# Optimization experiments

Hardware: AMD Instinct MI355X
Metric: run time of the kernel (lower is better)

## Reference

```python
import jax, jax.numpy as jnp
import numpy as np
import math

B, S, D, NH = 2, 2048, 1024, 16
DK = D // NH
E, TOPK, MOE_H, NSH = 8, 2, 1024, 2
SH_H = MOE_H * NSH
EPS = 1e-6


def setup_inputs() -> dict:
    key = jax.random.key(0)
    ks = jax.random.split(key, 24)
    p = lambda k, shape: jax.random.normal(k, shape, jnp.float32) * 0.02
    x = jax.random.normal(ks[0], (B, S, D), jnp.float32)
    # RoPE tables: freqs_cis = exp(i * t * theta^{-2j/dk}), passed as cos/sin
    inv = 1.0 / (10000.0 ** (np.arange(0, DK, 2, dtype=np.float32) / DK))
    ang = np.outer(np.arange(S, dtype=np.float32), inv)
    freqs_cos = jnp.asarray(np.cos(ang), jnp.float32)
    freqs_sin = jnp.asarray(np.sin(ang), jnp.float32)
    mask = jnp.triu(jnp.full((S, S), -1e9, jnp.float32), k=1)  # causal additive mask
    return {
        'x': x, 'freqs_cos': freqs_cos, 'freqs_sin': freqs_sin, 'mask': mask,
        'wq': p(ks[1], (D, D)), 'wk': p(ks[2], (D, D)),
        'wv': p(ks[3], (D, D)), 'wo': p(ks[4], (D, D)),
        'attn_norm_w': jnp.ones((D,), jnp.float32),
        'ffn_norm_w': jnp.ones((D,), jnp.float32),
        'gate_w': p(ks[5], (E, D)), 'gate_b': p(ks[6], (E,)),
        'w1': p(ks[7], (E, MOE_H, D)), 'b1': p(ks[8], (E, MOE_H)),
        'w2': p(ks[9], (E, D, MOE_H)), 'b2': p(ks[10], (E, D)),
        'w3': p(ks[11], (E, MOE_H, D)), 'b3': p(ks[12], (E, MOE_H)),
        'sg_w': p(ks[13], (SH_H, D)), 'su_w': p(ks[14], (SH_H, D)),
        'sd_w': p(ks[15], (D, SH_H)),
    }


def rmsnorm(x, w):
    f = x.astype(jnp.float32)
    y = f * jax.lax.rsqrt(jnp.mean(f * f, axis=-1, keepdims=True) + EPS)
    return y.astype(x.dtype) * w


def rope(t, cos, sin):
    # t: [b, s, h, dk]; pairs (t[2j], t[2j+1]) as complex, multiplied by e^{i ang}
    tr, ti = t[..., 0::2], t[..., 1::2]
    c, s = cos[None, :, None, :], sin[None, :, None, :]
    outr = tr * c - ti * s
    outi = tr * s + ti * c
    return jnp.stack([outr, outi], axis=-1).reshape(t.shape)


def reference(x, freqs_cos, freqs_sin, mask, wq, wk, wv, wo, attn_norm_w, ffn_norm_w,
              gate_w, gate_b, w1, b1, w2, b2, w3, b3, sg_w, su_w, sd_w):
    b, s, d = x.shape
    # --- attention with RoPE ---
    h = rmsnorm(x, attn_norm_w)
    q = (h @ wq.T).reshape(b, s, NH, DK)
    k = (h @ wk.T).reshape(b, s, NH, DK)
    v = (h @ wv.T).reshape(b, s, NH, DK)
    q = rope(q, freqs_cos, freqs_sin)
    k = rope(k, freqs_cos, freqs_sin)
    scale = 1.0 / math.sqrt(DK)
    q = q.transpose(0, 2, 1, 3)
    k = k.transpose(0, 2, 1, 3)
    v = v.transpose(0, 2, 1, 3)
    scores = jnp.einsum('bhqd,bhkd->bhqk', q, k) * scale + mask
    # NOTE: source divides by sqrt(d_k) a second time before softmax (faithful quirk)
    attn = jax.nn.softmax(scores * scale, axis=-1)
    o = jnp.einsum('bhqk,bhkd->bhqd', attn, v).transpose(0, 2, 1, 3).reshape(b, s, d)
    x = x + o @ wo.T
    # --- MoE FFN ---
    hf = rmsnorm(x, ffn_norm_w).reshape(-1, d)                 # [T, D]
    gscores = jax.nn.softmax(hf @ gate_w.T + gate_b, axis=-1)  # [T, E]
    _, idx = jax.lax.top_k(gscores, TOPK)                      # bias is None -> topk on scores
    weights = jnp.take_along_axis(gscores, idx, axis=1)        # original_scores gather
    wmask = (jax.nn.one_hot(idx, E, dtype=hf.dtype) * weights[..., None]).sum(1)  # [T, E]
    shared = (jax.nn.silu(hf @ sg_w.T) * (hf @ su_w.T)) @ sd_w.T
    a1 = jnp.einsum('td,ehd->teh', hf, w1) + b1
    a3 = jnp.einsum('td,ehd->teh', hf, w3) + b3
    eo = jnp.einsum('teh,edh->ted', jax.nn.silu(a1) * a3, w2) + b2  # [T, E, D]
    router = jnp.einsum('te,ted->td', wmask, eo)
    return x + (shared + router).reshape(x.shape)
```

## Files before the change

### kernel.cpp

```cpp
#include <hip/hip_runtime.h>


typedef unsigned short u16;
typedef __attribute__((ext_vector_type(8))) short bh8;
typedef __attribute__((ext_vector_type(4))) float fv4;
typedef __attribute__((ext_vector_type(4))) unsigned uv4;
typedef __attribute__((ext_vector_type(2))) int iv2;

#define LOG2E 1.4426950408889634f
#define MAX_TILES 71

__device__ __forceinline__ float b2f(u16 u) {
  return __builtin_bit_cast(float, ((unsigned)u) << 16);
}
__device__ __forceinline__ u16 f2b(float f) {
  unsigned x = __builtin_bit_cast(unsigned, f);
  return (u16)((x + 0x7fffu + ((x >> 16) & 1u)) >> 16);
}
__device__ __forceinline__ fv4 mfma16(bh8 a, bh8 b, fv4 c) {
  return __builtin_amdgcn_mfma_f32_16x16x32_bf16(a, b, c, 0, 0, 0);
}
__device__ __forceinline__ unsigned cvtpk(float lo, float hi) {
  unsigned r;
  asm("v_cvt_pk_bf16_f32 %0, %1, %2" : "=v"(r) : "v"(lo), "v"(hi));
  return r;
}

__device__ __forceinline__ void xcd_swizzle(int& bx, int& by) {
  int gx = gridDim.x;
  int nwg = gx * gridDim.y;
  int flat = by * gx + bx;
  int q = nwg >> 3, r = nwg & 7;
  int xcd = flat & 7, idx = flat >> 3;
  int swz = (xcd < r ? xcd * (q + 1) : r * (q + 1) + (xcd - r) * q) + idx;
  by = swz / gx;
  bx = swz - by * gx;
}
__device__ __forceinline__ int xcd_swizzle1d(int flat, int nwg) {
  int q = nwg >> 3, r = nwg & 7;
  int xcd = flat & 7, idx = flat >> 3;
  return (xcd < r ? xcd * (q + 1) : r * (q + 1) + (xcd - r) * q) + idx;
}

#define GLD16(g, l)                                                        \
  __builtin_amdgcn_global_load_lds(                                        \
      (const __attribute__((address_space(1))) void*)(g),                  \
      (__attribute__((address_space(3))) void*)(l), 16, 0, 0)

__device__ __forceinline__ bh8 lds_frag(const u16* base, int row, int b8) {
  int off = row * 128 + ((b8 * 16) ^ ((row & 7) << 4));
  return *(const bh8*)((const char*)base + off);
}

template <int MODE, int TM>
__device__ __forceinline__ void gemm_body(
    u16* AsB, u16* BsB, int bx, int by, const u16* __restrict__ A,
    const u16* __restrict__ B, int M, int N, int K, u16* __restrict__ Cb,
    float* __restrict__ Cf, const float* __restrict__ add1,
    const float* __restrict__ add2, const float* __restrict__ bias,
    const int* __restrict__ tmeta, const int* __restrict__ etok) {
  constexpr int MR = TM / 32;
  const int lane = threadIdx.x & 63;
  const int wid = threadIdx.x >> 6;
  const int wr = wid >> 1, wc = wid & 1;
  const int n0 = bx * 128;
  const int rr = lane >> 3;
  const int b8s = (lane & 7) ^ rr;
  const int ldA = (MODE == 6) ? M : K;

  int m0 = 0, e = 0, m0l = 0, cnt = 0, row0 = 0;
  const u16* Bp = B;
  if constexpr (MODE == 6 || MODE == 8) {
    int tile = by, half = 0;
    if constexpr (MODE == 6 && TM == 64) {
      tile = by >> 1;
      half = by & 1;
    }
    if (tile >= tmeta[0]) return;
    e = tmeta[16 + tile * 4];
    m0l = tmeta[17 + tile * 4];
    cnt = tmeta[18 + tile * 4];
    row0 = tmeta[19 + tile * 4] + half * 64;
    Bp = B + (size_t)e * N * K;
  } else {
    m0 = by * TM;
  }

  const u16* Arow[MR];
  const u16* Brow[4];
#pragma unroll
  for (int i = 0; i < MR; ++i) {
    int c = wid * MR + i;
    int row = c * 8 + rr;
    if constexpr (MODE == 8) {
      int li = m0l + row;
      li = li < cnt ? li : cnt - 1;
      int tok = etok[e * 4096 + li];
      Arow[i] = A + (size_t)tok * ldA + b8s * 8;
    } else if constexpr (MODE == 6) {
      Arow[i] = A + (size_t)(row0 + row) * ldA + b8s * 8;
    } else {
      Arow[i] = A + (size_t)(m0 + row) * ldA + b8s * 8;
    }
  }
#pragma unroll
  for (int i = 0; i < 4; ++i)
    Brow[i] = Bp + (size_t)(n0 + (wid * 4 + i) * 8 + rr) * K + b8s * 8;

  fv4 acc[MR][4] = {};
  const int nt = K >> 6;

#pragma unroll
  for (int i = 0; i < MR; ++i)
    GLD16(Arow[i], &AsB[(wid * MR + i) * 512]);
#pragma unroll
  for (int i = 0; i < 4; ++i)
    GLD16(Brow[i], &BsB[(wid * 4 + i) * 512]);

  for (int t = 0; t < nt; ++t) {
    const int cur = t & 1;
    u16* Asc = AsB + cur * (TM * 64);
    u16* Bsc = BsB + cur * (128 * 64);
    if (t + 1 < nt) {
      const int k0 = (t + 1) * 64;
      u16* Asn = AsB + (cur ^ 1) * (TM * 64);
      u16* Bsn = BsB + (cur ^ 1) * (128 * 64);
#pragma unroll
      for (int i = 0; i < MR; ++i)
        GLD16(Arow[i] + k0, &Asn[(wid * MR + i) * 512]);
#pragma unroll
      for (int i = 0; i < 4; ++i)
        GLD16(Brow[i] + k0, &Bsn[(wid * 4 + i) * 512]);
      if constexpr (MR == 4)
        asm volatile("s_waitcnt vmcnt(8)" ::: "memory");
      else
        asm volatile("s_waitcnt vmcnt(6)" ::: "memory");
    } else {
      asm volatile("s_waitcnt vmcnt(0)" ::: "memory");
    }
    __builtin_amdgcn_s_barrier();
    __builtin_amdgcn_sched_barrier(0);

#pragma unroll
    for (int ks = 0; ks < 2; ++ks) {
      int b8 = ks * 4 + (lane >> 4);
      bh8 af[MR], bf[4];
#pragma unroll
      for (int mi = 0; mi < MR; ++mi)
        af[mi] = lds_frag(Asc, wr * (16 * MR) + mi * 16 + (lane & 15), b8);
#pragma unroll
      for (int ni = 0; ni < 4; ++ni)
        bf[ni] = lds_frag(Bsc, wc * 64 + ni * 16 + (lane & 15), b8);
      __builtin_amdgcn_s_setprio(1);
#pragma unroll
      for (int mi = 0; mi < MR; ++mi)
#pragma unroll
        for (int ni = 0; ni < 4; ++ni)
          acc[mi][ni] = mfma16(af[mi], bf[ni], acc[mi][ni]);
      __builtin_amdgcn_s_setprio(0);
    }
    __builtin_amdgcn_sched_barrier(0);
    __builtin_amdgcn_s_barrier();
    __builtin_amdgcn_sched_barrier(0);
  }

  const int rbase = (MODE == 6 || MODE == 8) ? row0 : m0;
  const int r0b = rbase + wr * (16 * MR) + (lane >> 4) * 4;
  const int c0b = n0 + wc * 64 + (lane & 15);

  if constexpr (MODE == 7 || MODE == 8) {
    const int OUTN = N >> 1;
    const int colb = (n0 >> 1) + wc * 32;
    const float* bb1 = nullptr;
    const float* bb3 = nullptr;
    if constexpr (MODE == 8) {
      bb1 = add1 + (size_t)e * OUTN;
      bb3 = add2 + (size_t)e * OUTN;
    }
#pragma unroll
    for (int mi = 0; mi < MR; ++mi) {
#pragma unroll
      for (int ni = 0; ni < 2; ++ni) {
        int c = colb + ni * 16 + (lane & 15);
#pragma unroll
        for (int r = 0; r < 4; ++r) {
          int row = r0b + mi * 16 + r;
          float xg = acc[mi][ni][r];
          float yu = acc[mi][ni + 2][r];
          if constexpr (MODE == 8) {
            xg += bb1[c];
            yu += bb3[c];
          }
          float s = xg / (1.f + __expf(-xg));
          Cb[(size_t)row * OUTN + c] = f2b(s * yu);
        }
      }
    }
  } else if constexpr (MODE == 9) {
#pragma unroll
    for (int mi = 0; mi < MR; ++mi) {
#pragma unroll
      for (int r = 0; r < 4; ++r) {
        int row = r0b + mi * 16 + r;
        int g0 = tmeta[2 * row], g1 = tmeta[2 * row + 1];
        float w0 = bias[2 * row], w1 = bias[2 * row + 1];
        const u16* e0p = Cb + (size_t)g0 * 1024;
        const u16* e1p = Cb + (size_t)g1 * 1024;
#pragma unroll
        for (int ni = 0; ni < 4; ++ni) {
          int c = c0b + ni * 16;
          size_t idx = (size_t)row * N + c;
          Cf[idx] = add1[idx] + acc[mi][ni][r] + w0 * b2f(e0p[c]) +
                    w1 * b2f(e1p[c]);
        }
      }
    }
  } else {
    const float* bb = nullptr;
    if constexpr (MODE == 6) bb = bias + (size_t)e * N;
#pragma unroll
    for (int mi = 0; mi < MR; ++mi) {
#pragma unroll
      for (int ni = 0; ni < 4; ++ni) {
        int c = c0b + ni * 16;
#pragma unroll
        for (int r = 0; r < 4; ++r) {
          int row = r0b + mi * 16 + r;
          size_t idx = (size_t)row * N + c;
          float v = acc[mi][ni][r];
          if constexpr (MODE == 0) Cb[idx] = f2b(v);
          else if constexpr (MODE == 1) Cf[idx] = add1[idx] + v;
          else Cb[idx] = f2b(v + bb[c]);
        }
      }
    }
  }
}

template <int MODE, int TM = 128>
__global__ __launch_bounds__(256) void gemm_bt(
    const u16* __restrict__ A, const u16* __restrict__ B, int M, int N, int K,
    u16* __restrict__ Cb, float* __restrict__ Cf,
    const float* __restrict__ add1, const float* __restrict__ add2,
    const float* __restrict__ bias, const int* __restrict__ tmeta,
    const int* __restrict__ etok) {
  __shared__ u16 As[2][TM * 64];
  __shared__ u16 Bs[2][128 * 64];
  int bx = blockIdx.x, by = blockIdx.y;
  xcd_swizzle(bx, by);
  gemm_body<MODE, TM>(&As[0][0], &Bs[0][0], bx, by, A, B, M, N, K, Cb, Cf,
                      add1, add2, bias, tmeta, etok);
}

__global__ __launch_bounds__(256) void gemm_sgu_w13(
    const u16* __restrict__ hf, const u16* __restrict__ sgu_w,
    u16* __restrict__ hs, const u16* __restrict__ w13_w,
    u16* __restrict__ a13, const float* __restrict__ b1,
    const float* __restrict__ b3, const int* __restrict__ meta,
    const int* __restrict__ etok) {
  __shared__ u16 As[2][128 * 64];
  __shared__ u16 Bs[2][128 * 64];
  const int nwg = 1024 + 16 * MAX_TILES;
  int flat = xcd_swizzle1d((int)blockIdx.x, nwg);
  if (flat < 1024) {
    int by = flat >> 5, bx = flat & 31;
    gemm_body<7, 128>(&As[0][0], &Bs[0][0], bx, by, hf, sgu_w, 4096, 4096,
                      1024, hs, nullptr, nullptr, nullptr, nullptr, nullptr,
                      nullptr);
  } else {
    int idx = flat - 1024;
    int by = idx >> 4, bx = idx & 15;
    gemm_body<8, 128>(&As[0][0], &Bs[0][0], bx, by, hf, w13_w, 4096, 2048,
                      1024, a13, nullptr, b1, b3, nullptr, meta, etok);
  }
}

__global__ __launch_bounds__(256) void rmsnorm_bf16(
    const float* __restrict__ x, const float* __restrict__ w,
    u16* __restrict__ out) {
  int t = blockIdx.x;
  const float* xr = x + (size_t)t * 1024;
  fv4 v = *(const fv4*)(xr + threadIdx.x * 4);
  float ss = v[0] * v[0] + v[1] * v[1] + v[2] * v[2] + v[3] * v[3];
#pragma unroll
  for (int off = 1; off < 64; off <<= 1) ss += __shfl_xor(ss, off);
  __shared__ float red[4];
  int lane = threadIdx.x & 63, wid = threadIdx.x >> 6;
  if (lane == 0) red[wid] = ss;
  __syncthreads();
  float inv = rsqrtf((red[0] + red[1] + red[2] + red[3]) * (1.0f / 1024.f) + 1e-6f);
  u16* op = out + (size_t)t * 1024 + threadIdx.x * 4;
  const float* wp = w + threadIdx.x * 4;
#pragma unroll
  for (int i = 0; i < 4; ++i) op[i] = f2b(v[i] * inv * wp[i]);
}

__global__ __launch_bounds__(256) void rope_repack(
    const u16* __restrict__ qkv, const float* __restrict__ fc,
    const float* __restrict__ fs, u16* __restrict__ qr, u16* __restrict__ kr,
    u16* __restrict__ vt, int S) {
  __shared__ u16 tile[64][65];
  const int s0 = blockIdx.x * 64;
  const int b = blockIdx.y;
  const int h0 = blockIdx.z * 4;
#pragma unroll 4
  for (int it = 0; it < 32; ++it) {
    int idx = threadIdx.x + it * 256;
    int tl = idx >> 7, rem = idx & 127;
    int h = h0 + (rem >> 5), i = rem & 31;
    int s = s0 + tl;
    float c = fc[s * 32 + i], sn = fs[s * 32 + i];
    size_t src = ((size_t)(b * S + s)) * 3072 + h * 64 + 2 * i;
    size_t dst = ((size_t)((b * 16 + h) * S + s)) * 64 + 2 * i;
    float a0 = b2f(qkv[src]), a1 = b2f(qkv[src + 1]);
    qr[dst] = f2b(a0 * c - a1 * sn);
    qr[dst + 1] = f2b(a0 * sn + a1 * c);
    float b0 = b2f(qkv[src + 1024]), b1 = b2f(qkv[src + 1025]);
    kr[dst] = f2b(b0 * c - b1 * sn);
    kr[dst + 1] = f2b(b0 * sn + b1 * c);
  }
  for (int hh = 0; hh < 4; ++hh) {
    int h = h0 + hh;
    __syncthreads();
    for (int cc = threadIdx.x; cc < 512; cc += 256) {
      int tl = cc >> 3, d8 = cc & 7;
      bh8 val = *(const bh8*)(qkv + ((size_t)(b * S + s0 + tl)) * 3072 + 2048 +
                              h * 64 + d8 * 8);
#pragma unroll
      for (int j = 0; j < 8; ++j) tile[tl][d8 * 8 + j] = (u16)val[j];
    }
    __syncthreads();
    for (int cc = threadIdx.x; cc < 512; cc += 256) {
      int d = cc >> 3, pg = cc & 7;
      int sbase = 16 * (pg >> 2) + 4 * (pg & 3);
      bh8 o;
#pragma unroll
      for (int j = 0; j < 8; ++j)
        o[j] = (short)tile[sbase + (j & 3) + ((j >> 2) << 5)][d];
      *(bh8*)(vt + ((size_t)((b * 16 + h) * 64 + d)) * S + s0 + pg * 8) = o;
    }
  }
}

__global__ __launch_bounds__(256) void attn_fwd(
    const u16* __restrict__ qr, const u16* __restrict__ kr,
    const u16* __restrict__ vt, u16* __restrict__ ob, int S, int NHc) {
  __shared__ u16 Ks[2][64 * 64];
  __shared__ u16 Vs[2][64 * 64];
  const int lane = threadIdx.x & 63;
  const int wid = threadIdx.x >> 6;
  const int g = lane >> 4;
  const int l15 = lane & 15;
  const int bh = blockIdx.x;
  const int ia = blockIdx.y;
  const int nq = S / 64;
  const int qa0 = ia * 64;
  const int qb0 = (nq - 1 - ia) * 64;
  const int b = bh / NHc, h = bh % NHc;
  const u16* qbase = qr + (size_t)bh * S * 64;
  const u16* kb = kr + (size_t)bh * S * 64;
  const u16* vb = vt + (size_t)bh * 64 * S;
  const float SC = 0.015625f * LOG2E;
  const int rr = lane >> 3;
  const int b8s = (lane & 7) ^ rr;

  bh8 ONES;
#pragma unroll
  for (int j = 0; j < 8; ++j) ONES[j] = (short)0x3f80;

  bh8 qfA[2], qfB[2];
  {
    const u16* qp = qbase + (size_t)(qa0 + wid * 16 + l15) * 64 + g * 8;
    qfA[0] = *(const bh8*)qp;
    qfA[1] = *(const bh8*)(qp + 32);
    qp = qbase + (size_t)(qb0 + wid * 16 + l15) * 64 + g * 8;
    qfB[0] = *(const bh8*)qp;
    qfB[1] = *(const bh8*)(qp + 32);
  }
  fv4 oaccA[4] = {}, oaccB[4] = {};
  fv4 lA = {}, lB = {};
  float mA = -1e30f, mB = -1e30f;
  const int nktB = nq - ia;

  auto stage = [&](int buf, int j0) {
#pragma unroll
    for (int i = 0; i < 2; ++i) {
      int c = wid * 2 + i;
      int row = c * 8 + rr;
      GLD16(kb + (size_t)(j0 + row) * 64 + b8s * 8, &Ks[buf][c * 512]);
      GLD16(vb + (size_t)row * S + j0 + b8s * 8, &Vs[buf][c * 512]);
    }
  };
  stage(0, 0);

  auto process = [&](const bh8 (&kf)[2][4], const bh8 (&vf)[2][4], int j0,
                     int q0x, bh8* qf, fv4* oacc, float& mrow, fv4& lrowC) {
    const int q_my = q0x + wid * 16 + l15;
    fv4 st[4] = {};
    __builtin_amdgcn_s_setprio(1);
#pragma unroll
    for (int ks = 0; ks < 2; ++ks)
#pragma unroll
      for (int jt = 0; jt < 4; ++jt)
        st[jt] = mfma16(kf[ks][jt], qf[ks], st[jt]);
    __builtin_amdgcn_s_setprio(0);

    float sr[4][4];
    float mloc = -1e30f;
    const int jb = j0 + 4 * g;
    if (j0 + 63 > q0x + wid * 16) {
#pragma unroll
      for (int jt = 0; jt < 4; ++jt)
#pragma unroll
        for (int r = 0; r < 4; ++r) {
          int j = jb + jt * 16 + r;
          float s = (j <= q_my) ? st[jt][r] : -1e30f;
          sr[jt][r] = s;
          mloc = fmaxf(mloc, s);
        }
    } else {
#pragma unroll
      for (int jt = 0; jt < 4; ++jt)
#pragma unroll
        for (int r = 0; r < 4; ++r) {
          sr[jt][r] = st[jt][r];
          mloc = fmaxf(mloc, st[jt][r]);
        }
    }
    mloc = fmaxf(mloc, __shfl_xor(mloc, 16));
    mloc = fmaxf(mloc, __shfl_xor(mloc, 32));
    mloc *= SC;
    bool defer = __all(mloc <= mrow + 8.f);
    if (!defer) {
      float mnew = fmaxf(mrow, mloc);
      float sfac = exp2f(mrow - mnew);
      mrow = mnew;
      float sfC[4];
#pragma unroll
      for (int r = 0; r < 4; ++r) sfC[r] = __shfl(sfac, g * 4 + r);
#pragma unroll
      for (int dt = 0; dt < 4; ++dt)
#pragma unroll
        for (int r = 0; r < 4; ++r) oacc[dt][r] *= sfC[r];
#pragma unroll
      for (int r = 0; r < 4; ++r) lrowC[r] *= sfC[r];
    }
    float p[4][4];
#pragma unroll
    for (int jt = 0; jt < 4; ++jt)
#pragma unroll
      for (int r = 0; r < 4; ++r)
        p[jt][r] = exp2f(fmaf(sr[jt][r], SC, -mrow));

    __builtin_amdgcn_s_setprio(1);
    fv4 racc = {};
#pragma unroll
    for (int ks = 0; ks < 2; ++ks) {
      uv4 w;
      w[0] = cvtpk(p[ks][0], p[ks][1]);
      w[1] = cvtpk(p[ks][2], p[ks][3]);
      w[2] = cvtpk(p[ks + 2][0], p[ks + 2][1]);
      w[3] = cvtpk(p[ks + 2][2], p[ks + 2][3]);
      bh8 pa = __builtin_bit_cast(bh8, w);
      racc = mfma16(pa, ONES, racc);
#pragma unroll
      for (int dt = 0; dt < 4; ++dt)
        oacc[dt] = mfma16(pa, vf[ks][dt], oacc[dt]);
    }
    __builtin_amdgcn_s_setprio(0);
#pragma unroll
    for (int r = 0; r < 4; ++r) lrowC[r] += racc[r];
  };

  for (int kt = 0; kt < nktB; ++kt) {
    const int j0 = kt * 64;
    __syncthreads();
    if (kt + 1 < nktB) stage((kt + 1) & 1, (kt + 1) * 64);
    const u16* Kc = Ks[kt & 1];
    const u16* Vc = Vs[kt & 1];
    bh8 kf[2][4], vf[2][4];
#pragma unroll
    for (int ks = 0; ks < 2; ++ks) {
      int b8 = ks * 4 + g;
#pragma unroll
      for (int jt = 0; jt < 4; ++jt)
        kf[ks][jt] = lds_frag(Kc, jt * 16 + l15, b8);
#pragma unroll
      for (int dt = 0; dt < 4; ++dt)
        vf[ks][dt] = lds_frag(Vc, dt * 16 + l15, b8);
    }
    process(kf, vf, j0, qb0, qfB, oaccB, mB, lB);
    if (kt <= ia) process(kf, vf, j0, qa0, qfA, oaccA, mA, lA);
  }

  auto wout = [&](fv4* oacc, fv4 lrowC, int q0x) {
#pragma unroll
    for (int dt = 0; dt < 4; ++dt)
#pragma unroll
      for (int r = 0; r < 4; ++r) {
        int row = q0x + wid * 16 + g * 4 + r;
        int col = dt * 16 + l15;
        ob[((size_t)b * S + row) * 1024 + h * 64 + col] =
            f2b(oacc[dt][r] / lrowC[r]);
      }
  };
  wout(oaccA, lA, qa0);
  wout(oaccB, lB, qb0);
}

__global__ __launch_bounds__(256) void gate_topk(
    const float* __restrict__ x2, const float* __restrict__ nw,
    const float* __restrict__ gw, const float* __restrict__ gb,
    int* __restrict__ topk_e, float* __restrict__ topk_w,
    u16* __restrict__ hf) {
  int t = blockIdx.x * 4 + (threadIdx.x >> 6);
  int lane = threadIdx.x & 63;
  const float* xr = x2 + (size_t)t * 1024;
  float hv[16];
  float ss = 0.f;
#pragma unroll
  for (int i = 0; i < 4; ++i) {
    fv4 v = *(const fv4*)(xr + lane * 16 + i * 4);
#pragma unroll
    for (int j = 0; j < 4; ++j) {
      hv[i * 4 + j] = v[j];
      ss += v[j] * v[j];
    }
  }
#pragma unroll
  for (int off = 1; off < 64; off <<= 1) ss += __shfl_xor(ss, off);
  float inv = rsqrtf(ss * (1.0f / 1024.f) + 1e-6f);
  const fv4* nwp = (const fv4*)(nw + lane * 16);
#pragma unroll
  for (int i = 0; i < 4; ++i) {
    fv4 wv = nwp[i];
#pragma unroll
    for (int j = 0; j < 4; ++j) hv[i * 4 + j] *= inv * wv[j];
  }
  {
    bh8 o0, o1;
#pragma unroll
    for (int j = 0; j < 8; ++j) {
      o0[j] = (short)f2b(hv[j]);
      o1[j] = (short)f2b(hv[8 + j]);
    }
    u16* hp = hf + (size_t)t * 1024 + lane * 16;
    *(bh8*)hp = o0;
    *(bh8*)(hp + 8) = o1;
  }
  float logit[8];
#pragma unroll
  for (int e = 0; e < 8; ++e) {
    const fv4* wp = (const fv4*)(gw + (size_t)e * 1024 + lane * 16);
    float s = 0.f;
#pragma unroll
    for (int i = 0; i < 4; ++i) {
      fv4 wv = wp[i];
#pragma unroll
      for (int j = 0; j < 4; ++j) s += hv[i * 4 + j] * wv[j];
    }
    logit[e] = s;
  }
#pragma unroll
  for (int off = 1; off < 64; off <<= 1)
#pragma unroll
    for (int e = 0; e < 8; ++e) logit[e] += __shfl_xor(logit[e], off);
  if (lane == 0) {
#pragma unroll
    for (int e = 0; e < 8; ++e) logit[e] += gb[e];
    float mx = logit[0];
#pragma unroll
    for (int e = 1; e < 8; ++e) mx = fmaxf(mx, logit[e]);
    float pe[8], se = 0.f;
#pragma unroll
    for (int e = 0; e < 8; ++e) { pe[e] = __expf(logit[e] - mx); se += pe[e]; }
    float rs = 1.f / se;
#pragma unroll
    for (int e = 0; e < 8; ++e) pe[e] *= rs;
    int i0 = 0;
    float b0 = pe[0];
#pragma unroll
    for (int e = 1; e < 8; ++e)
      if (pe[e] > b0) { b0 = pe[e]; i0 = e; }
    int i1 = -1;
    float b1v = -1.f;
#pragma unroll
    for (int e = 0; e < 8; ++e)
      if (e != i0 && pe[e] > b1v) { b1v = pe[e]; i1 = e; }
    topk_e[2 * t] = i0;
    topk_e[2 * t + 1] = i1;
    topk_w[2 * t] = b0;
    topk_w[2 * t + 1] = b1v;
  }
}

__global__ __launch_bounds__(512) void route_tokens(
    const int* __restrict__ topk_e, int* __restrict__ pos_of,
    int* __restrict__ etok, int* __restrict__ meta, int* __restrict__ rowid,
    int T2) {
  __shared__ int scnt[8], sbase[8];
  const int e = threadIdx.x >> 6;
  const int lane = threadIdx.x & 63;
  int base = 0;
  for (int i0 = 0; i0 < T2; i0 += 128) {
    iv2 te = *(const iv2*)(topk_e + i0 + lane * 2);
    unsigned long long m0 = __ballot(te[0] == e);
    unsigned long long m1 = __ballot(te[1] == e);
    unsigned long long lt = (1ull << lane) - 1;
    int pre = __popcll(m0 & lt) + __popcll(m1 & lt);
    if (te[0] == e) {
      int pos = base + pre;
      etok[e * 4096 + pos] = (i0 >> 1) + lane;
      pos_of[i0 + lane * 2] = pos;
      ++pre;
    }
    if (te[1] == e) {
      int pos = base + pre;
      etok[e * 4096 + pos] = (i0 >> 1) + lane;
      pos_of[i0 + lane * 2 + 1] = pos;
    }
    base += __popcll(m0) + __popcll(m1);
  }
  if (lane == 0) scnt[e] = base;
  __syncthreads();
  if (threadIdx.x == 0) {
    int tt = 0, rb = 0;
#pragma unroll
    for (int e2 = 0; e2 < 8; ++e2) {
      sbase[e2] = rb;
      int c = scnt[e2];
      int nt = (c + 127) >> 7;
      for (int i = 0; i < nt; ++i) {
        meta[16 + tt * 4] = e2;
        meta[17 + tt * 4] = i * 128;
        meta[18 + tt * 4] = c;
        meta[19 + tt * 4] = rb + i * 128;
        ++tt;
      }
      rb += nt * 128;
    }
    meta[0] = tt;
  }
  __syncthreads();
  for (int i = threadIdx.x; i < T2; i += 512)
    rowid[i] = sbase[topk_e[i]] + pos_of[i];
}

__global__ __launch_bounds__(256) void f2b_convert(
    const float* __restrict__ src, u16* __restrict__ dst) {
  size_t i = ((size_t)blockIdx.x * 256 + threadIdx.x) * 8;
  fv4 a = *(const fv4*)(src + i);
  fv4 b = *(const fv4*)(src + i + 4);
  bh8 o;
#pragma unroll
  for (int j = 0; j < 4; ++j) o[j] = (short)f2b(a[j]);
#pragma unroll
  for (int j = 0; j < 4; ++j) o[4 + j] = (short)f2b(b[j]);
  *(bh8*)(dst + i) = o;
}

__global__ __launch_bounds__(256) void f2b_convert_ilv(
    const float* __restrict__ src, u16* __restrict__ dst, int half,
    int seg_shift) {
  size_t i = ((size_t)blockIdx.x * 256 + threadIdx.x) * 8;
  int r = (int)(i >> 10), col = (int)(i & 1023);
  int rl = r & ((1 << seg_shift) - 1), e = r >> seg_shift;
  int dstrow = (e << (seg_shift + 1)) + ((rl >> 5) << 6) + (rl & 31) +
               (half << 5);
  fv4 a = *(const fv4*)(src + i);
  fv4 b = *(const fv4*)(src + i + 4);
  bh8 o;
#pragma unroll
  for (int j = 0; j < 4; ++j) o[j] = (short)f2b(a[j]);
#pragma unroll
  for (int j = 0; j < 4; ++j) o[4 + j] = (short)f2b(b[j]);
  *(bh8*)(dst + (size_t)dstrow * 1024 + col) = o;
}

extern "C" void kernel_launch(void* const* d_in, const int* in_sizes, int n_in,
                              void* d_out, int out_size, void* d_ws,
                              size_t ws_size, hipStream_t stream) {
  (void)in_sizes; (void)n_in; (void)out_size; (void)ws_size;
  const int Sc = 2048, Dc = 1024, NHc = 16, Tc = 4096, SH = 2048;

  const float* x   = (const float*)d_in[0];
  const float* fc  = (const float*)d_in[1];
  const float* fs  = (const float*)d_in[2];
  const float* wq  = (const float*)d_in[4];
  const float* wk  = (const float*)d_in[5];
  const float* wv  = (const float*)d_in[6];
  const float* wo  = (const float*)d_in[7];
  const float* anw = (const float*)d_in[8];
  const float* fnw = (const float*)d_in[9];
  const float* gw  = (const float*)d_in[10];
  const float* gb  = (const float*)d_in[11];
  const float* w1  = (const float*)d_in[12];
  const float* b1  = (const float*)d_in[13];
  const float* w2  = (const float*)d_in[14];
  const float* b2  = (const float*)d_in[15];
  const float* w3  = (const float*)d_in[16];
  const float* b3  = (const float*)d_in[17];
  const float* sgw = (const float*)d_in[18];
  const float* suw = (const float*)d_in[19];
  const float* sdw = (const float*)d_in[20];
  float* out = (float*)d_out;

  char* base = (char*)d_ws;
  size_t off = 0;
  auto alloc = [&](size_t bytes) -> void* {
    void* p = base + off;
    off += (bytes + 255) & ~(size_t)255;
    return p;
  };
  u16* wqkv_b = (u16*)alloc(2ull * 3072 * 1024);
  u16* wo_b   = (u16*)alloc(2ull * 1024 * 1024);
  u16* sgu_b  = (u16*)alloc(2ull * 4096 * 1024);
  u16* sdw_b  = (u16*)alloc(2ull * 1024 * 2048);
  u16* w13_b  = (u16*)alloc(2ull * 8 * 2048 * 1024);
  u16* w2_b   = (u16*)alloc(2ull * 8 * 1024 * 1024);
  char* regA = (char*)alloc(2ull * Tc * 4096);
  char* regB = (char*)alloc(2ull * (size_t)MAX_TILES * 128 * 2048);
  float* x2  = (float*)alloc(4ull * Tc * Dc);
  u16* hs_b  = (u16*)alloc(2ull * Tc * SH);
  int* topk_e = (int*)alloc(2ull * Tc * 4);
  float* topk_w = (float*)alloc(2ull * Tc * 4);
  int* pos_of = (int*)alloc(2ull * Tc * 4);
  int* rowid = (int*)alloc(2ull * Tc * 4);
  int* etok = (int*)alloc(8ull * 4096 * 4);
  int* meta = (int*)alloc(512 * 4);

  u16* qkv_out = (u16*)regA;
  u16* eo_c    = (u16*)regA;
  u16* h_b  = (u16*)regB;
  u16* qr   = (u16*)regB;
  u16* kr   = (u16*)(regB + 2ull * Tc * Dc);
  u16* vt_  = (u16*)(regB + 4ull * Tc * Dc);
  u16* o_b  = (u16*)(regB + 6ull * Tc * Dc);
  u16* a13_c = (u16*)regB;
  u16* hf_b = wqkv_b;

  auto conv = [&](const float* s, u16* d, size_t n) {
    f2b_convert<<<dim3((unsigned)(n / 2048)), 256, 0, stream>>>(s, d);
  };
  conv(wq, wqkv_b, (size_t)Dc * Dc);
  conv(wk, wqkv_b + 1048576, (size_t)Dc * Dc);
  conv(wv, wqkv_b + 2097152, (size_t)Dc * Dc);
  conv(wo, wo_b, (size_t)Dc * Dc);
  conv(sdw, sdw_b, (size_t)Dc * SH);
  conv(w2, w2_b, 8ull * 1024 * 1024);
  f2b_convert_ilv<<<1024, 256, 0, stream>>>(sgw, sgu_b, 0, 11);
  f2b_convert_ilv<<<1024, 256, 0, stream>>>(suw, sgu_b, 1, 11);
  f2b_convert_ilv<<<4096, 256, 0, stream>>>(w1, w13_b, 0, 10);
  f2b_convert_ilv<<<4096, 256, 0, stream>>>(w3, w13_b, 1, 10);

  rmsnorm_bf16<<<Tc, 256, 0, stream>>>(x, anw, h_b);
  gemm_bt<0><<<dim3(3072 / 128, Tc / 128), 256, 0, stream>>>(
      h_b, wqkv_b, Tc, 3072, Dc, qkv_out, nullptr, nullptr, nullptr, nullptr,
      nullptr, nullptr);
  rope_repack<<<dim3(Sc / 64, 2, 4), 256, 0, stream>>>(qkv_out, fc, fs, qr, kr,
                                                       vt_, Sc);
  attn_fwd<<<dim3(2 * NHc, Sc / 128), 256, 0, stream>>>(qr, kr, vt_, o_b, Sc,
                                                        NHc);
  gemm_bt<1, 64><<<dim3(Dc / 128, Tc / 64), 256, 0, stream>>>(
      o_b, wo_b, Tc, Dc, Dc, nullptr, x2, x, nullptr, nullptr, nullptr,
      nullptr);

  gate_topk<<<Tc / 4, 256, 0, stream>>>(x2, fnw, gw, gb, topk_e, topk_w,
                                        hf_b);
  route_tokens<<<1, 512, 0, stream>>>(topk_e, pos_of, etok, meta, rowid,
                                      2 * Tc);

  gemm_sgu_w13<<<dim3(1024 + 16 * MAX_TILES), 256, 0, stream>>>(
      hf_b, sgu_b, hs_b, w13_b, a13_c, b1, b3, meta, etok);

  gemm_bt<6, 64><<<dim3(Dc / 128, 2 * MAX_TILES), 256, 0, stream>>>(
      a13_c, w2_b, 1024, Dc, 1024, eo_c, nullptr, nullptr, nullptr,
      b2, meta, etok);

  gemm_bt<9, 64><<<dim3(Dc / 128, Tc / 64), 256, 0, stream>>>(
      hs_b, sdw_b, Tc, Dc, SH, eo_c, out, x2, nullptr, topk_w, rowid,
      nullptr);
}
```

Before: 398.2 us.

## Add supertile block ordering to GEMMs and double-size KV staging in attention

```diff
diff --git a/kernel.cpp b/kernel.cpp
--- a/kernel.cpp
+++ b/kernel.cpp
@@ -26,16 +26,6 @@
   return r;
 }
 
-__device__ __forceinline__ void xcd_swizzle(int& bx, int& by) {
-  int gx = gridDim.x;
-  int nwg = gx * gridDim.y;
-  int flat = by * gx + bx;
-  int q = nwg >> 3, r = nwg & 7;
-  int xcd = flat & 7, idx = flat >> 3;
-  int swz = (xcd < r ? xcd * (q + 1) : r * (q + 1) + (xcd - r) * q) + idx;
-  by = swz / gx;
-  bx = swz - by * gx;
-}
 __device__ __forceinline__ int xcd_swizzle1d(int flat, int nwg) {
   int q = nwg >> 3, r = nwg & 7;
   int xcd = flat & 7, idx = flat >> 3;
@@ -237,7 +227,7 @@
   }
 }
 
-template <int MODE, int TM = 128>
+template <int MODE, int TM = 128, int STILE = 0>
 __global__ __launch_bounds__(256) void gemm_bt(
     const u16* __restrict__ A, const u16* __restrict__ B, int M, int N, int K,
     u16* __restrict__ Cb, float* __restrict__ Cf,
@@ -246,8 +236,20 @@
     const int* __restrict__ etok) {
   __shared__ u16 As[2][TM * 64];
   __shared__ u16 Bs[2][128 * 64];
-  int bx = blockIdx.x, by = blockIdx.y;
-  xcd_swizzle(bx, by);
+  const int gx = gridDim.x;
+  int flat = (int)blockIdx.y * gx + (int)blockIdx.x;
+  flat = xcd_swizzle1d(flat, gx * (int)gridDim.y);
+  int bx, by;
+  if constexpr (STILE) {
+    int SX = gx >> 2;
+    int sidx = flat >> 5, within = flat & 31;
+    int sy = sidx / SX, sx = sidx - sy * SX;
+    by = sy * 8 + (within >> 2);
+    bx = sx * 4 + (within & 3);
+  } else {
+    by = flat / gx;
+    bx = flat - by * gx;
+  }
   gemm_body<MODE, TM>(&As[0][0], &Bs[0][0], bx, by, A, B, M, N, K, Cb, Cf,
                       add1, add2, bias, tmeta, etok);
 }
@@ -263,7 +265,10 @@
   const int nwg = 1024 + 16 * MAX_TILES;
   int flat = xcd_swizzle1d((int)blockIdx.x, nwg);
   if (flat < 1024) {
-    int by = flat >> 5, bx = flat & 31;
+    int sidx = flat >> 5, within = flat & 31;
+    int sy = sidx >> 3, sx = sidx & 7;
+    int by = sy * 8 + (within >> 2);
+    int bx = sx * 4 + (within & 3);
     gemm_body<7, 128>(&As[0][0], &Bs[0][0], bx, by, hf, sgu_w, 4096, 4096,
                       1024, hs, nullptr, nullptr, nullptr, nullptr, nullptr,
                       nullptr);
@@ -345,8 +350,8 @@
 __global__ __launch_bounds__(256) void attn_fwd(
     const u16* __restrict__ qr, const u16* __restrict__ kr,
     const u16* __restrict__ vt, u16* __restrict__ ob, int S, int NHc) {
-  __shared__ u16 Ks[2][64 * 64];
-  __shared__ u16 Vs[2][64 * 64];
+  __shared__ u16 Ks[2][2][64 * 64];
+  __shared__ u16 Vs[2][2][64 * 64];
   const int lane = threadIdx.x & 63;
   const int wid = threadIdx.x >> 6;
   const int g = lane >> 4;
@@ -381,17 +386,22 @@
   fv4 lA = {}, lB = {};
   float mA = -1e30f, mB = -1e30f;
   const int nktB = nq - ia;
-
-  auto stage = [&](int buf, int j0) {
-#pragma unroll
-    for (int i = 0; i < 2; ++i) {
-      int c = wid * 2 + i;
-      int row = c * 8 + rr;
-      GLD16(kb + (size_t)(j0 + row) * 64 + b8s * 8, &Ks[buf][c * 512]);
-      GLD16(vb + (size_t)row * S + j0 + b8s * 8, &Vs[buf][c * 512]);
+  const int nrounds = (nktB + 1) >> 1;
+
+  auto stage = [&](int buf, int j0, int nsub) {
+    for (int s = 0; s < nsub; ++s) {
+#pragma unroll
+      for (int i = 0; i < 2; ++i) {
+        int c = wid * 2 + i;
+        int row = c * 8 + rr;
+        GLD16(kb + (size_t)(j0 + s * 64 + row) * 64 + b8s * 8,
+              &Ks[buf][s][c * 512]);
+        GLD16(vb + (size_t)row * S + j0 + s * 64 + b8s * 8,
+              &Vs[buf][s][c * 512]);
+      }
     }
   };
-  stage(0, 0);
+  stage(0, 0, nktB > 1 ? 2 : 1);
 
   auto process = [&](const bh8 (&kf)[2][4], const bh8 (&vf)[2][4], int j0,
                      int q0x, bh8* qf, fv4* oacc, float& mrow, fv4& lrowC) {
@@ -472,25 +482,31 @@
     for (int r = 0; r < 4; ++r) lrowC[r] += racc[r];
   };
 
-  for (int kt = 0; kt < nktB; ++kt) {
-    const int j0 = kt * 64;
+  for (int rd = 0; rd < nrounds; ++rd) {
     __syncthreads();
-    if (kt + 1 < nktB) stage((kt + 1) & 1, (kt + 1) * 64);
-    const u16* Kc = Ks[kt & 1];
-    const u16* Vc = Vs[kt & 1];
-    bh8 kf[2][4], vf[2][4];
-#pragma unroll
-    for (int ks = 0; ks < 2; ++ks) {
-      int b8 = ks * 4 + g;
-#pragma unroll
-      for (int jt = 0; jt < 4; ++jt)
-        kf[ks][jt] = lds_frag(Kc, jt * 16 + l15, b8);
-#pragma unroll
-      for (int dt = 0; dt < 4; ++dt)
-        vf[ks][dt] = lds_frag(Vc, dt * 16 + l15, b8);
-    }
-    process(kf, vf, j0, qb0, qfB, oaccB, mB, lB);
-    if (kt <= ia) process(kf, vf, j0, qa0, qfA, oaccA, mA, lA);
+    int rem = nktB - (rd + 1) * 2;
+    if (rem > 0) stage((rd + 1) & 1, (rd + 1) * 128, rem > 1 ? 2 : 1);
+#pragma unroll
+    for (int s = 0; s < 2; ++s) {
+      int kt = rd * 2 + s;
+      if (kt >= nktB) break;
+      const int j0 = kt * 64;
+      const u16* Kc = Ks[rd & 1][s];
+      const u16* Vc = Vs[rd & 1][s];
+      bh8 kf[2][4], vf[2][4];
+#pragma unroll
+      for (int ks = 0; ks < 2; ++ks) {
+        int b8 = ks * 4 + g;
+#pragma unroll
+        for (int jt = 0; jt < 4; ++jt)
+          kf[ks][jt] = lds_frag(Kc, jt * 16 + l15, b8);
+#pragma unroll
+        for (int dt = 0; dt < 4; ++dt)
+          vf[ks][dt] = lds_frag(Vc, dt * 16 + l15, b8);
+      }
+      process(kf, vf, j0, qb0, qfB, oaccB, mB, lB);
+      if (kt <= ia) process(kf, vf, j0, qa0, qfA, oaccA, mA, lA);
+    }
   }
 
   auto wout = [&](fv4* oacc, fv4 lrowC, int q0x) {
@@ -754,14 +770,14 @@
   f2b_convert_ilv<<<4096, 256, 0, stream>>>(w3, w13_b, 1, 10);
 
   rmsnorm_bf16<<<Tc, 256, 0, stream>>>(x, anw, h_b);
-  gemm_bt<0><<<dim3(3072 / 128, Tc / 128), 256, 0, stream>>>(
+  gemm_bt<0, 128, 1><<<dim3(3072 / 128, Tc / 128), 256, 0, stream>>>(
       h_b, wqkv_b, Tc, 3072, Dc, qkv_out, nullptr, nullptr, nullptr, nullptr,
       nullptr, nullptr);
   rope_repack<<<dim3(Sc / 64, 2, 4), 256, 0, stream>>>(qkv_out, fc, fs, qr, kr,
                                                        vt_, Sc);
   attn_fwd<<<dim3(2 * NHc, Sc / 128), 256, 0, stream>>>(qr, kr, vt_, o_b, Sc,
                                                         NHc);
-  gemm_bt<1, 64><<<dim3(Dc / 128, Tc / 64), 256, 0, stream>>>(
+  gemm_bt<1, 64, 1><<<dim3(Dc / 128, Tc / 64), 256, 0, stream>>>(
       o_b, wo_b, Tc, Dc, Dc, nullptr, x2, x, nullptr, nullptr, nullptr,
       nullptr);
 
@@ -777,7 +793,7 @@
       a13_c, w2_b, 1024, Dc, 1024, eo_c, nullptr, nullptr, nullptr,
       b2, meta, etok);
 
-  gemm_bt<9, 64><<<dim3(Dc / 128, Tc / 64), 256, 0, stream>>>(
+  gemm_bt<9, 64, 1><<<dim3(Dc / 128, Tc / 64), 256, 0, stream>>>(
       hs_b, sdw_b, Tc, Dc, SH, eo_c, out, x2, nullptr, topk_w, rowid,
       nullptr);
 }
```

After: 398.3 us. Within noise of the previous version (+0.0%).
